# Performance work log

Hardware: AMD Instinct MI355X
Metric: run time of the kernel (lower is better)

The kernel has to match this reference:

```python
import jax, jax.numpy as jnp
import numpy as np

GROUPS = 32
EPS = 1e-5

def group_norm(x, w, b):
    # x: [B, C, T]
    B, C, T = x.shape
    g = x.reshape(B, GROUPS, C // GROUPS, T)
    mu = g.mean(axis=(2, 3), keepdims=True)
    var = g.var(axis=(2, 3), keepdims=True)
    g = (g - mu) * jax.lax.rsqrt(var + EPS)
    return g.reshape(B, C, T) * w[None, :, None] + b[None, :, None]

def conv1x1(x, w, b):
    # x: [B, C, T], w: [O, C], b: [O]
    return jnp.einsum('oc,bct->bot', w, x) + b[None, :, None]

def setup_inputs() -> dict:
    key = jax.random.key(0)
    ks = jax.random.split(key, 10)
    B, C, H, W = 128, 512, 16, 16
    d = {}
    d['criminal_cond'] = jax.random.normal(ks[0], (B, C, H, W), jnp.float32)
    d['morph_cond'] = jax.random.normal(ks[1], (B, C, H, W), jnp.float32)
    d['norm_w'] = jax.random.uniform(ks[2], (C,), jnp.float32, 0.5, 1.5)
    d['norm_b'] = 0.02 * jax.random.normal(ks[3], (C,), jnp.float32)
    d['qkv_w'] = jax.random.normal(ks[4], (3 * C, C), jnp.float32) / np.sqrt(C)
    d['qkv_b'] = 0.02 * jax.random.normal(ks[5], (3 * C,), jnp.float32)
    d['ekv_w'] = jax.random.normal(ks[6], (2 * C, C), jnp.float32) / np.sqrt(C)
    d['ekv_b'] = 0.02 * jax.random.normal(ks[7], (2 * C,), jnp.float32)
    d['proj_w'] = jax.random.normal(ks[8], (C, C), jnp.float32) / np.sqrt(C)
    d['proj_b'] = 0.02 * jax.random.normal(ks[9], (C,), jnp.float32)
    return d

def reference(criminal_cond, morph_cond, norm_w, norm_b, qkv_w, qkv_b, ekv_w, ekv_b, proj_w, proj_b):
    B, C, H, W = criminal_cond.shape
    x = criminal_cond.reshape(B, C, H * W)          # [B, C, T]
    cond = morph_cond.reshape(B, C, H * W)          # [B, C, S], S == T here
    h = group_norm(x, norm_w, norm_b)
    qkv = conv1x1(h, qkv_w, qkv_b)                  # [B, 3C, T]
    q, k, v = jnp.split(qkv, 3, axis=1)
    ekv = conv1x1(cond, ekv_w, ekv_b)               # [B, 2C, S]
    ek, ev = jnp.split(ekv, 2, axis=1)
    k = jnp.concatenate([ek, k], axis=-1)           # [B, C, S+T]
    v = jnp.concatenate([ev, v], axis=-1)
    scale = 1.0 / np.sqrt(np.sqrt(C))               # single head, head_dim = C
    logits = jnp.einsum('bct,bcs->bts', q * scale, k * scale)
    w = jax.nn.softmax(logits, axis=-1)             # [B, T, S+T]
    a = jnp.einsum('bts,bcs->bct', w, v)            # [B, C, T]
    hout = conv1x1(a, proj_w, proj_b)
    attn_out = (x + hout).reshape(B, C, H, W)
    return 2.0 * morph_cond - attn_out
```

## Files before the change

### kernel.cpp

```cpp
#include <hip/hip_runtime.h>
#include <hip/hip_bf16.h>
#include <math.h>

#define NB 128
#define NC 512
#define NT 256
#define NL 512
#define NG 32
#define SCALE2 0.04419417382415922f

typedef __attribute__((ext_vector_type(8))) short bf16x8;
typedef __attribute__((ext_vector_type(4))) float f32x4;
typedef __attribute__((ext_vector_type(4))) unsigned short u16x4;
typedef __hip_bfloat16 bf16;

struct Params {
  const float *x, *morph, *qkvb, *ekvb, *projb;
  const bf16 *wq, *we, *wp;
  bf16 *hT, *mT, *qT, *kfT, *vf, *pr, *aT;
  float *out;
  int b0;
};

enum { M_QKV = 0, M_EKV = 1, M_LOG = 2, M_PV = 3, M_PROJ = 4 };

__device__ inline unsigned short f2bf_bits(float f) {
  bf16 h = __float2bfloat16(f);
  return *reinterpret_cast<unsigned short*>(&h);
}

__global__ __launch_bounds__(256) void gn_stats_k(const float* __restrict__ x,
                                                  float* __restrict__ stats) {
  const int bg = blockIdx.x;
  const float* p = x + (size_t)bg * 4096;
  float s = 0.f, s2 = 0.f;
  for (int i = threadIdx.x; i < 4096; i += 256) {
    float v = p[i];
    s += v; s2 += v * v;
  }
  for (int off = 32; off; off >>= 1) {
    s  += __shfl_down(s, off);
    s2 += __shfl_down(s2, off);
  }
  __shared__ float red[8];
  const int wave = threadIdx.x >> 6, lane = threadIdx.x & 63;
  if (lane == 0) { red[wave * 2] = s; red[wave * 2 + 1] = s2; }
  __syncthreads();
  if (threadIdx.x == 0) {
    float S = 0.f, S2 = 0.f;
    for (int w = 0; w < 4; ++w) { S += red[w * 2]; S2 += red[w * 2 + 1]; }
    float mu = S * (1.0f / 4096.0f);
    float var = S2 * (1.0f / 4096.0f) - mu * mu;
    stats[bg * 2]     = mu;
    stats[bg * 2 + 1] = rsqrtf(var + 1e-5f);
  }
}

__global__ __launch_bounds__(256) void cvt_k(const float* __restrict__ s,
                                             bf16* __restrict__ d, int n) {
  int i = blockIdx.x * 256 + threadIdx.x;
  if (i < n) d[i] = __float2bfloat16(s[i]);
}

template <int NORM>
__global__ __launch_bounds__(256) void transpose_k(const float* __restrict__ src,
                                                   bf16* __restrict__ dst,
                                                   const float* __restrict__ stats,
                                                   const float* __restrict__ gnw,
                                                   const float* __restrict__ gnb,
                                                   int b0) {
  __shared__ float sm[32][33];
  const int lb = blockIdx.z, gb = b0 + lb;
  const int c0 = blockIdx.y * 32, t0 = blockIdx.x * 32;
  const int tx = threadIdx.x & 31, ty = threadIdx.x >> 5;
  const float* s = src + ((size_t)gb * NC + c0) * NT + t0;
  #pragma unroll
  for (int j = 0; j < 4; ++j) {
    int c = ty + j * 8;
    float v = s[c * NT + tx];
    if (NORM) {
      int cg = c0 + c;
      float mu = stats[(gb * NG + (cg >> 4)) * 2];
      float rs = stats[(gb * NG + (cg >> 4)) * 2 + 1];
      v = (v - mu) * rs * gnw[cg] + gnb[cg];
    }
    sm[c][tx] = v;
  }
  __syncthreads();
  bf16* d = dst + ((size_t)lb * NT + t0) * NC + c0;
  #pragma unroll
  for (int j = 0; j < 4; ++j)
    d[(size_t)(ty + j * 8) * NC + tx] = __float2bfloat16(sm[tx][ty + j * 8]);
}

template <int MODE>
__global__ __launch_bounds__(256) void gemm_k(Params P) {
  __shared__ unsigned short As[128][40];
  __shared__ unsigned short Bs[128][40];
  const int lb = blockIdx.z, gb = P.b0 + lb;
  const int m0 = blockIdx.y * 128;
  const int n0 = blockIdx.x * 128;
  const int tid = threadIdx.x;
  const int lane = tid & 63, w = tid >> 6;
  const int wr = w >> 1, wc = w & 1;
  const int ln = lane & 15, kq = lane >> 4;

  const bf16 *Ab, *Bb;
  if (MODE == M_QKV)      { Ab = P.hT + (size_t)lb * NT * NC; Bb = P.wq; }
  else if (MODE == M_EKV) { Ab = P.mT + (size_t)lb * NT * NC; Bb = P.we; }
  else if (MODE == M_LOG) { Ab = P.qT + (size_t)lb * NT * NC; Bb = P.kfT + (size_t)lb * NL * NC; }
  else if (MODE == M_PV)  { Ab = P.pr + (size_t)lb * NT * NL; Bb = P.vf + (size_t)lb * NC * NL; }
  else                    { Ab = P.aT + (size_t)lb * NT * NC; Bb = P.wp; }

  const uint4* Ag = (const uint4*)(Ab + (size_t)m0 * 512);
  const uint4* Bg = (const uint4*)(Bb + (size_t)n0 * 512);

  f32x4 acc[4][4] = {};

  for (int k0 = 0; k0 < 512; k0 += 32) {
    const int kb = k0 >> 3;
    #pragma unroll
    for (int h = 0; h < 2; ++h) {
      int ch = tid + h * 256;
      int row = ch >> 2, cid = ch & 3;
      *(uint4*)&As[row][cid * 8] = Ag[row * 64 + kb + cid];
      *(uint4*)&Bs[row][cid * 8] = Bg[row * 64 + kb + cid];
    }
    __syncthreads();
    bf16x8 af[4], bfr[4];
    #pragma unroll
    for (int i = 0; i < 4; ++i)
      af[i] = *(const bf16x8*)&As[wr * 64 + i * 16 + ln][kq * 8];
    #pragma unroll
    for (int j = 0; j < 4; ++j)
      bfr[j] = *(const bf16x8*)&Bs[wc * 64 + j * 16 + ln][kq * 8];
    #pragma unroll
    for (int i = 0; i < 4; ++i)
      #pragma unroll
      for (int j = 0; j < 4; ++j)
        acc[i][j] = __builtin_amdgcn_mfma_f32_16x16x32_bf16(af[i], bfr[j], acc[i][j], 0, 0, 0);
    __syncthreads();
  }

  #pragma unroll
  for (int i = 0; i < 4; ++i) {
    const int ig = m0 + wr * 64 + i * 16 + kq * 4;
    #pragma unroll
    for (int j = 0; j < 4; ++j) {
      const int jg = n0 + wc * 64 + j * 16 + ln;
      f32x4 a = acc[i][j];
      if (MODE == M_QKV) {
        float bias = P.qkvb[jg];
        if (jg < 512) {
          bf16* d = P.qT + ((size_t)lb * NT + ig) * NC + jg;
          #pragma unroll
          for (int r = 0; r < 4; ++r) d[(size_t)r * NC] = __float2bfloat16(a[r] + bias);
        } else if (jg < 1024) {
          bf16* d = P.kfT + ((size_t)lb * NL + 256 + ig) * NC + (jg - 512);
          #pragma unroll
          for (int r = 0; r < 4; ++r) d[(size_t)r * NC] = __float2bfloat16(a[r] + bias);
        } else {
          u16x4 pk;
          #pragma unroll
          for (int r = 0; r < 4; ++r) pk[r] = f2bf_bits(a[r] + bias);
          *(u16x4*)(P.vf + ((size_t)lb * NC + (jg - 1024)) * NL + 256 + ig) = pk;
        }
      } else if (MODE == M_EKV) {
        float bias = P.ekvb[jg];
        if (jg < 512) {
          bf16* d = P.kfT + ((size_t)lb * NL + ig) * NC + jg;
          #pragma unroll
          for (int r = 0; r < 4; ++r) d[(size_t)r * NC] = __float2bfloat16(a[r] + bias);
        } else {
          u16x4 pk;
          #pragma unroll
          for (int r = 0; r < 4; ++r) pk[r] = f2bf_bits(a[r] + bias);
          *(u16x4*)(P.vf + ((size_t)lb * NC + (jg - 512)) * NL + ig) = pk;
        }
      } else if (MODE == M_LOG) {
        bf16* d = P.pr + ((size_t)lb * NT + ig) * NL + jg;
        #pragma unroll
        for (int r = 0; r < 4; ++r) d[(size_t)r * NL] = __float2bfloat16(a[r] * SCALE2);
      } else if (MODE == M_PV) {
        bf16* d = P.aT + ((size_t)lb * NT + ig) * NC + jg;
        #pragma unroll
        for (int r = 0; r < 4; ++r) d[(size_t)r * NC] = __float2bfloat16(a[r]);
      } else {
        float bias = P.projb[jg];
        const size_t idx = ((size_t)gb * NC + jg) * NT + ig;
        float4 mo = *(const float4*)&P.morph[idx];
        float4 xx = *(const float4*)&P.x[idx];
        f32x4 o;
        o[0] = 2.0f * mo.x - xx.x - (a[0] + bias);
        o[1] = 2.0f * mo.y - xx.y - (a[1] + bias);
        o[2] = 2.0f * mo.z - xx.z - (a[2] + bias);
        o[3] = 2.0f * mo.w - xx.w - (a[3] + bias);
        *(f32x4*)&P.out[idx] = o;
      }
    }
  }
}

__global__ __launch_bounds__(256) void softmax_k(bf16* __restrict__ pr) {
  const size_t row = (size_t)blockIdx.x * 4 + (threadIdx.x >> 6);
  const int lane = threadIdx.x & 63;
  bf16* p = pr + row * NL + lane * 8;
  float v[8];
  float m = -1e30f;
  #pragma unroll
  for (int i = 0; i < 8; ++i) {
    v[i] = __bfloat162float(p[i]);
    m = fmaxf(m, v[i]);
  }
  #pragma unroll
  for (int off = 32; off; off >>= 1) m = fmaxf(m, __shfl_xor(m, off));
  float s = 0.f;
  #pragma unroll
  for (int i = 0; i < 8; ++i) { v[i] = __expf(v[i] - m); s += v[i]; }
  #pragma unroll
  for (int off = 32; off; off >>= 1) s += __shfl_xor(s, off);
  const float inv = 1.0f / s;
  #pragma unroll
  for (int i = 0; i < 8; ++i) p[i] = __float2bfloat16(v[i] * inv);
}

extern "C" void kernel_launch(void* const* d_in, const int* in_sizes, int n_in,
                              void* d_out, int out_size, void* d_ws, size_t ws_size,
                              hipStream_t stream) {
  const float* x     = (const float*)d_in[0];
  const float* morph = (const float*)d_in[1];
  const float* gnw   = (const float*)d_in[2];
  const float* gnb   = (const float*)d_in[3];
  const float* qkvw  = (const float*)d_in[4];
  const float* qkvb  = (const float*)d_in[5];
  const float* ekvw  = (const float*)d_in[6];
  const float* ekvb  = (const float*)d_in[7];
  const float* projw = (const float*)d_in[8];
  const float* projb = (const float*)d_in[9];

  bf16* wq = (bf16*)d_ws;
  bf16* we = wq + 786432;
  bf16* wp = we + 524288;
  float* stats = (float*)(wp + 262144);
  bf16* pb = (bf16*)(stats + 8192);

  const size_t per_b = 1179648;
  const size_t fixed = (size_t)(786432 + 524288 + 262144) * 2 + 8192 * 4;
  int nbc = NB;
  while (nbc > 1 && fixed + (size_t)nbc * per_b * 2 > ws_size) nbc >>= 1;

  Params P;
  P.x = x; P.morph = morph; P.qkvb = qkvb; P.ekvb = ekvb; P.projb = projb;
  P.wq = wq; P.we = we; P.wp = wp;
  P.hT  = pb;                         pb += (size_t)nbc * 131072;
  P.mT  = pb;                         pb += (size_t)nbc * 131072;
  P.qT  = pb;                         pb += (size_t)nbc * 131072;
  P.kfT = pb;                         pb += (size_t)nbc * 262144;
  P.vf  = pb;                         pb += (size_t)nbc * 262144;
  P.pr  = pb;                         pb += (size_t)nbc * 131072;
  P.aT  = pb;
  P.out = (float*)d_out;

  gn_stats_k<<<dim3(NB * NG), dim3(256), 0, stream>>>(x, stats);
  cvt_k<<<dim3(3072), dim3(256), 0, stream>>>(qkvw, wq, 786432);
  cvt_k<<<dim3(2048), dim3(256), 0, stream>>>(ekvw, we, 524288);
  cvt_k<<<dim3(1024), dim3(256), 0, stream>>>(projw, wp, 262144);

  for (int b0 = 0; b0 < NB; b0 += nbc) {
    P.b0 = b0;
    transpose_k<1><<<dim3(8, 16, nbc), dim3(256), 0, stream>>>(x, P.hT, stats, gnw, gnb, b0);
    transpose_k<0><<<dim3(8, 16, nbc), dim3(256), 0, stream>>>(morph, P.mT, stats, gnw, gnb, b0);
    gemm_k<M_QKV> <<<dim3(12, 2, nbc), dim3(256), 0, stream>>>(P);
    gemm_k<M_EKV> <<<dim3(8, 2, nbc),  dim3(256), 0, stream>>>(P);
    gemm_k<M_LOG> <<<dim3(4, 2, nbc),  dim3(256), 0, stream>>>(P);
    softmax_k     <<<dim3(nbc * 64),   dim3(256), 0, stream>>>(P.pr);
    gemm_k<M_PV>  <<<dim3(4, 2, nbc),  dim3(256), 0, stream>>>(P);
    gemm_k<M_PROJ><<<dim3(4, 2, nbc),  dim3(256), 0, stream>>>(P);
  }
}
```

Baseline: 603.6 us.

## Use direct global-to-LDS loads in GEMM, fuse transposes, alias workspace buffers

The GEMM tile loads now use global_load_lds to copy 16-byte chunks straight into unpadded LDS. This skips the register round trip for each tile load. The two transpose kernels are merged into one launch, and the pr/aT buffers now reuse the mT/hT storage, which shrinks workspace per batch and may allow larger batch chunks. Dropping the LDS padding can bring back bank conflicts on the fragment reads. The buffer aliasing is only safe because of stream ordering.

```diff
diff --git a/kernel.cpp b/kernel.cpp
--- a/kernel.cpp
+++ b/kernel.cpp
@@ -27,6 +27,12 @@
 __device__ inline unsigned short f2bf_bits(float f) {
   bf16 h = __float2bfloat16(f);
   return *reinterpret_cast<unsigned short*>(&h);
+}
+
+__device__ inline void gld16(const void* g, void* lds) {
+  __builtin_amdgcn_global_load_lds(
+      (const __attribute__((address_space(1))) unsigned int*)g,
+      (__attribute__((address_space(3))) unsigned int*)lds, 16, 0, 0);
 }
 
 __global__ __launch_bounds__(256) void gn_stats_k(const float* __restrict__ x,
@@ -62,15 +68,21 @@
   if (i < n) d[i] = __float2bfloat16(s[i]);
 }
 
-template <int NORM>
-__global__ __launch_bounds__(256) void transpose_k(const float* __restrict__ src,
-                                                   bf16* __restrict__ dst,
-                                                   const float* __restrict__ stats,
-                                                   const float* __restrict__ gnw,
-                                                   const float* __restrict__ gnb,
-                                                   int b0) {
+__global__ __launch_bounds__(256) void transpose2_k(const float* __restrict__ x,
+                                                    const float* __restrict__ morph,
+                                                    bf16* __restrict__ hT,
+                                                    bf16* __restrict__ mT,
+                                                    const float* __restrict__ stats,
+                                                    const float* __restrict__ gnw,
+                                                    const float* __restrict__ gnb,
+                                                    int b0, int nbc) {
   __shared__ float sm[32][33];
-  const int lb = blockIdx.z, gb = b0 + lb;
+  const int z = blockIdx.z;
+  const int norm = (z < nbc) ? 1 : 0;
+  const int lb = norm ? z : z - nbc;
+  const int gb = b0 + lb;
+  const float* src = norm ? x : morph;
+  bf16* dst = norm ? hT : mT;
   const int c0 = blockIdx.y * 32, t0 = blockIdx.x * 32;
   const int tx = threadIdx.x & 31, ty = threadIdx.x >> 5;
   const float* s = src + ((size_t)gb * NC + c0) * NT + t0;
@@ -78,7 +90,7 @@
   for (int j = 0; j < 4; ++j) {
     int c = ty + j * 8;
     float v = s[c * NT + tx];
-    if (NORM) {
+    if (norm) {
       int cg = c0 + c;
       float mu = stats[(gb * NG + (cg >> 4)) * 2];
       float rs = stats[(gb * NG + (cg >> 4)) * 2 + 1];
@@ -95,8 +107,8 @@
 
 template <int MODE>
 __global__ __launch_bounds__(256) void gemm_k(Params P) {
-  __shared__ unsigned short As[128][40];
-  __shared__ unsigned short Bs[128][40];
+  __shared__ unsigned short As[128][32];
+  __shared__ unsigned short Bs[128][32];
   const int lb = blockIdx.z, gb = P.b0 + lb;
   const int m0 = blockIdx.y * 128;
   const int n0 = blockIdx.x * 128;
@@ -112,19 +124,21 @@
   else if (MODE == M_PV)  { Ab = P.pr + (size_t)lb * NT * NL; Bb = P.vf + (size_t)lb * NC * NL; }
   else                    { Ab = P.aT + (size_t)lb * NT * NC; Bb = P.wp; }
 
-  const uint4* Ag = (const uint4*)(Ab + (size_t)m0 * 512);
-  const uint4* Bg = (const uint4*)(Bb + (size_t)n0 * 512);
+  const char* Abase = (const char*)(Ab + (size_t)m0 * 512);
+  const char* Bbase = (const char*)(Bb + (size_t)n0 * 512);
+
+  const int r_lo = w * 32 + (lane >> 2);
+  const int cid16 = (lane & 3) * 16;
 
   f32x4 acc[4][4] = {};
 
   for (int k0 = 0; k0 < 512; k0 += 32) {
-    const int kb = k0 >> 3;
+    const size_t kb = (size_t)k0 * 2 + cid16;
     #pragma unroll
     for (int h = 0; h < 2; ++h) {
-      int ch = tid + h * 256;
-      int row = ch >> 2, cid = ch & 3;
-      *(uint4*)&As[row][cid * 8] = Ag[row * 64 + kb + cid];
-      *(uint4*)&Bs[row][cid * 8] = Bg[row * 64 + kb + cid];
+      const int rw = r_lo + h * 16;
+      gld16(Abase + (size_t)rw * 1024 + kb, (char*)As + w * 2048 + h * 1024);
+      gld16(Bbase + (size_t)rw * 1024 + kb, (char*)Bs + w * 2048 + h * 1024);
     }
     __syncthreads();
     bf16x8 af[4], bfr[4];
@@ -244,7 +258,7 @@
   float* stats = (float*)(wp + 262144);
   bf16* pb = (bf16*)(stats + 8192);
 
-  const size_t per_b = 1179648;
+  const size_t per_b = 917504;
   const size_t fixed = (size_t)(786432 + 524288 + 262144) * 2 + 8192 * 4;
   int nbc = NB;
   while (nbc > 1 && fixed + (size_t)nbc * per_b * 2 > ws_size) nbc >>= 1;
@@ -256,9 +270,9 @@
   P.mT  = pb;                         pb += (size_t)nbc * 131072;
   P.qT  = pb;                         pb += (size_t)nbc * 131072;
   P.kfT = pb;                         pb += (size_t)nbc * 262144;
-  P.vf  = pb;                         pb += (size_t)nbc * 262144;
-  P.pr  = pb;                         pb += (size_t)nbc * 131072;
-  P.aT  = pb;
+  P.vf  = pb;
+  P.pr  = P.mT;
+  P.aT  = P.hT;
   P.out = (float*)d_out;
 
   gn_stats_k<<<dim3(NB * NG), dim3(256), 0, stream>>>(x, stats);
@@ -268,8 +282,8 @@
 
   for (int b0 = 0; b0 < NB; b0 += nbc) {
     P.b0 = b0;
-    transpose_k<1><<<dim3(8, 16, nbc), dim3(256), 0, stream>>>(x, P.hT, stats, gnw, gnb, b0);
-    transpose_k<0><<<dim3(8, 16, nbc), dim3(256), 0, stream>>>(morph, P.mT, stats, gnw, gnb, b0);
+    transpose2_k<<<dim3(8, 16, 2 * nbc), dim3(256), 0, stream>>>(
+        x, morph, P.hT, P.mT, stats, gnw, gnb, b0, nbc);
     gemm_k<M_QKV> <<<dim3(12, 2, nbc), dim3(256), 0, stream>>>(P);
     gemm_k<M_EKV> <<<dim3(8, 2, nbc),  dim3(256), 0, stream>>>(P);
     gemm_k<M_LOG> <<<dim3(4, 2, nbc),  dim3(256), 0, stream>>>(P);
```

Measured after the change: 583.7 us. 3.3% less time.
